# Kernel optimization log

Measured on AMD Instinct MI355X. Metric: run time of the kernel, lower is better.

Reference implementation:

```python
import jax, jax.numpy as jnp
import numpy as np

N_NODES = 100000
N_EDGES = 1600000
D_IN = 128
D_OUT = 128


def setup_inputs() -> dict:
    key = jax.random.key(0)
    k = jax.random.split(key, 7)
    x = jax.random.normal(k[0], (N_NODES, D_IN), dtype=jnp.float32)
    edge_index = jax.random.randint(k[1], (2, N_EDGES), 0, N_NODES, dtype=jnp.int32)
    # MLP params (PyTorch Linear-style scaling)
    s1 = 1.0 / np.sqrt(D_IN)
    s2 = 1.0 / np.sqrt(D_OUT)
    W1 = jax.random.uniform(k[2], (D_IN, D_OUT), jnp.float32, -s1, s1)
    b1 = jax.random.uniform(k[3], (D_OUT,), jnp.float32, -s1, s1)
    W2 = jax.random.uniform(k[4], (D_OUT, D_OUT), jnp.float32, -s2, s2)
    b2 = jax.random.uniform(k[5], (D_OUT,), jnp.float32, -s2, s2)
    eps = jnp.zeros((), dtype=jnp.float32)  # train_eps=True, init 0
    return {"x": x, "edge_index": edge_index, "W1": W1, "b1": b1, "W2": W2, "b2": b2, "eps": eps}


def reference(x, edge_index, W1, b1, W2, b2, eps):
    src, dst = edge_index[0], edge_index[1]  # flow: source_to_target
    # scatter-add neighbor aggregation: agg[i] = sum_{(j->i)} x[j]
    agg = jax.ops.segment_sum(x[src], dst, num_segments=x.shape[0])  # [N, D_IN]
    h = (1.0 + eps) * x + agg
    # 2-layer MLP: Linear -> ReLU -> Linear
    h = jax.nn.relu(h @ W1 + b1)
    return h @ W2 + b2
```

## Files before the change

### kernel.cpp

```cpp
#include <hip/hip_runtime.h>

#define NN    100000
#define NE    1600000
#define DD    128
#define CAP   64
#define NBKT  391
#define PCAP  4608
#define EPB   4096

typedef float  f4v __attribute__((ext_vector_type(4)));
typedef short  s8v __attribute__((ext_vector_type(8)));
typedef unsigned short u16;
typedef unsigned int   u32;

static __device__ __forceinline__ u16 f2bf(float f) {
    u32 u = __float_as_uint(f);
    return (u16)((u + 0x7fffu + ((u >> 16) & 1u)) >> 16);
}
static __device__ __forceinline__ float blo(u32 p) { return __uint_as_float(p << 16); }
static __device__ __forceinline__ float bhi(u32 p) { return __uint_as_float(p & 0xffff0000u); }

__global__ __launch_bounds__(256) void prep_cvt(
    const float* __restrict__ x,
    const float* __restrict__ W1, const float* __restrict__ W2,
    u32* __restrict__ xbp, u16* __restrict__ img1, u16* __restrict__ img2,
    int* __restrict__ gcnt)
{
    const int b   = blockIdx.x;
    const int tid = threadIdx.x;
    if (b < 25000) {
        const int row  = b * 4 + (tid >> 6);
        const int lane = tid & 63;
        const float* xp = x + (size_t)row * DD;
        xbp[(size_t)row * 64 + lane] =
            (u32)f2bf(xp[lane]) | ((u32)f2bf(xp[lane + 64]) << 16);
    } else if (b < 25008) {
        const int gid  = (b - 25000) * 256 + tid;
        const int frag = gid >> 6;
        const int lane = gid & 63;
        const int n  = (frag >> 2) * 16 + (lane & 15);
        const int k0 = (frag & 3) * 32 + (lane >> 4) * 8;
        u16* o1 = img1 + (size_t)gid * 8;
        u16* o2 = img2 + (size_t)gid * 8;
#pragma unroll
        for (int j = 0; j < 8; ++j) {
            o1[j] = f2bf(W1[(size_t)(k0 + j) * DD + n]);
            o2[j] = f2bf(W2[(size_t)(k0 + j) * DD + n]);
        }
    } else if (b < 25033) {
        const int i = (b - 25008) * 256 + tid;
        if (i < NBKT * 16) gcnt[i] = 0;
    } else {
        if (tid < 64) xbp[(size_t)NN * 64 + tid] = 0;
    }
}

__global__ __launch_bounds__(256) void part_kernel(
    const int* __restrict__ ei, u32* __restrict__ pairs, int* __restrict__ gcnt)
{
    __shared__ int hist[NBKT];
    __shared__ int base[NBKT];
    const int tid = threadIdx.x;
    const int e0  = blockIdx.x * EPB;

    int sv[16], dv[16];
#pragma unroll
    for (int t = 0; t < 16; ++t) {
        const int e = e0 + t * 256 + tid;
        if (e < NE) { sv[t] = ei[e]; dv[t] = ei[NE + e]; }
        else        { dv[t] = -1; sv[t] = 0; }
    }

    for (int i = tid; i < NBKT; i += 256) hist[i] = 0;
    __syncthreads();

#pragma unroll
    for (int t = 0; t < 16; ++t)
        if (dv[t] >= 0) atomicAdd(&hist[dv[t] >> 8], 1);
    __syncthreads();

    for (int i = tid; i < NBKT; i += 256) {
        const int h = hist[i];
        base[i] = h ? atomicAdd(&gcnt[i * 16], h) : 0;
        hist[i] = 0;
    }
    __syncthreads();

#pragma unroll
    for (int t = 0; t < 16; ++t)
        if (dv[t] >= 0) {
            const int bk = dv[t] >> 8;
            const int r  = base[bk] + atomicAdd(&hist[bk], 1);
            if (r < PCAP)
                pairs[(size_t)bk * PCAP + r] = ((u32)sv[t] << 8) | (u32)(dv[t] & 255);
        }
}

__global__ __launch_bounds__(256) void build_kernel(
    const u32* __restrict__ pairs, const int* __restrict__ gcnt,
    int* __restrict__ cnt, int* __restrict__ eidx)
{
    __shared__ int cl[256], cur[256];
    const int b   = blockIdx.x;
    const int tid = threadIdx.x;
    const int n   = min(gcnt[b * 16], PCAP);
    const u32* pp = pairs + (size_t)b * PCAP;

    u32 pv[18];
#pragma unroll
    for (int t = 0; t < 18; ++t) {
        const int i = t * 256 + tid;
        if (i < n) pv[t] = pp[i];
    }

    cl[tid] = 0; cur[tid] = 0;
    __syncthreads();

#pragma unroll
    for (int t = 0; t < 18; ++t) {
        const int i = t * 256 + tid;
        if (i < n) atomicAdd(&cl[pv[t] & 255], 1);
    }
    __syncthreads();

    const int g = b * 256 + tid;
    if (g < NN) cnt[g] = cl[tid];

#pragma unroll
    for (int t = 0; t < 18; ++t) {
        const int i = t * 256 + tid;
        if (i < n) {
            const u32 p  = pv[t];
            const int ld = p & 255;
            const int r  = atomicAdd(&cur[ld], 1);
            if (r < CAP) eidx[(size_t)(b * 256 + ld) * CAP + r] = (int)(p >> 8);
        }
    }
}

__global__ __launch_bounds__(256) void gather_kernel(
    const u32* __restrict__ xbp, const int* __restrict__ cnt,
    const int* __restrict__ eidx, const float* __restrict__ epsp,
    u16* __restrict__ hb)
{
    const int node = blockIdx.x * 4 + (threadIdx.x >> 6);
    const int lane = threadIdx.x & 63;
    const int deg  = min(cnt[node], CAP);

    int idxv = eidx[(size_t)node * CAP + lane];
    if (lane >= deg) idxv = NN;

    float a[4] = {}, c[4] = {};

    auto batch16 = [&](int j) {
        u32 p[16];
#pragma unroll
        for (int t = 0; t < 16; ++t) {
            const int s = __builtin_amdgcn_readlane(idxv, j + t);
            const u32* row = xbp + ((size_t)(u32)s << 6);
            p[t] = row[lane];
        }
#pragma unroll
        for (int t = 0; t < 16; ++t) { a[t & 3] += blo(p[t]); c[t & 3] += bhi(p[t]); }
    };
    auto batch8 = [&](int j) {
        u32 p[8];
#pragma unroll
        for (int t = 0; t < 8; ++t) {
            const int s = __builtin_amdgcn_readlane(idxv, j + t);
            const u32* row = xbp + ((size_t)(u32)s << 6);
            p[t] = row[lane];
        }
#pragma unroll
        for (int t = 0; t < 8; ++t) { a[t & 3] += blo(p[t]); c[t & 3] += bhi(p[t]); }
    };

    int j = 0;
    for (; j + 16 <= deg; j += 16) batch16(j);
    const int rem = deg - j;
    if (rem > 0) {
        if (rem <= 8) batch8(j);
        else          batch16(j);
    }

    const float sc = 1.0f + epsp[0];
    const u32 ps = xbp[(size_t)node * 64 + lane];
    const float r0 = sc * blo(ps) + ((a[0] + a[1]) + (a[2] + a[3]));
    const float r1 = sc * bhi(ps) + ((c[0] + c[1]) + (c[2] + c[3]));
    hb[(size_t)node * DD + lane]      = f2bf(r0);
    hb[(size_t)node * DD + lane + 64] = f2bf(r1);
}

__global__ __launch_bounds__(256) void mlp_kernel(
    const u16* __restrict__ hb,
    const u16* __restrict__ img1, const u16* __restrict__ img2,
    const float* __restrict__ b1, const float* __restrict__ b2,
    float* __restrict__ out)
{
    __shared__ char lds_raw[4 * 8448];
    const int tid  = threadIdx.x;
    const int wave = tid >> 6;
    const int lane = tid & 63;
    const int l15  = lane & 15;
    const int quad = lane >> 4;

    float* fstage = (float*)(lds_raw + wave * 8448);
    u16*   hstage = (u16*)fstage;

    int rbase = (blockIdx.x * 4 + wave) * 16;
    if (rbase > NN - 16) rbase = NN - 16;

    float bv1[8], bv2[8];
#pragma unroll
    for (int nt = 0; nt < 8; ++nt) {
        bv1[nt] = b1[nt * 16 + l15];
        bv2[nt] = b2[nt * 16 + l15];
    }

    s8v afrag[4];
#pragma unroll
    for (int kc = 0; kc < 4; ++kc)
        afrag[kc] = *(const s8v*)(hb + (size_t)(rbase + l15) * DD + kc * 32 + quad * 8);

    f4v acc1[8] = {};
#pragma unroll
    for (int kc = 0; kc < 4; ++kc)
#pragma unroll
        for (int nt = 0; nt < 8; ++nt) {
            const s8v bfr = *(const s8v*)(img1 + ((size_t)((nt * 4 + kc) * 64 + lane)) * 8);
            acc1[nt] = __builtin_amdgcn_mfma_f32_16x16x32_bf16(afrag[kc], bfr, acc1[nt], 0, 0, 0);
        }

#pragma unroll
    for (int nt = 0; nt < 8; ++nt)
#pragma unroll
        for (int r = 0; r < 4; ++r) {
            const float v = fmaxf(acc1[nt][r] + bv1[nt], 0.0f);
            hstage[(quad * 4 + r) * 136 + nt * 16 + l15] = f2bf(v);
        }
    __syncthreads();

    s8v a2[4];
#pragma unroll
    for (int kc = 0; kc < 4; ++kc)
        a2[kc] = *(const s8v*)&hstage[l15 * 136 + kc * 32 + quad * 8];

    f4v acc2[8] = {};
#pragma unroll
    for (int kc = 0; kc < 4; ++kc)
#pragma unroll
        for (int nt = 0; nt < 8; ++nt) {
            const s8v bfr = *(const s8v*)(img2 + ((size_t)((nt * 4 + kc) * 64 + lane)) * 8);
            acc2[nt] = __builtin_amdgcn_mfma_f32_16x16x32_bf16(a2[kc], bfr, acc2[nt], 0, 0, 0);
        }

    __syncthreads();
#pragma unroll
    for (int nt = 0; nt < 8; ++nt)
#pragma unroll
        for (int r = 0; r < 4; ++r)
            fstage[(quad * 4 + r) * 132 + nt * 16 + l15] = acc2[nt][r] + bv2[nt];
    __syncthreads();

#pragma unroll
    for (int i = 0; i < 8; ++i) {
        const int m  = (lane >> 5) + 2 * i;
        const int c4 = lane & 31;
        const f4v v = *(const f4v*)&fstage[m * 132 + c4 * 4];
        *(f4v*)(out + (size_t)(rbase + m) * DD + c4 * 4) = v;
    }
}

extern "C" void kernel_launch(void* const* d_in, const int* in_sizes, int n_in,
                              void* d_out, int out_size, void* d_ws, size_t ws_size,
                              hipStream_t stream) {
    const float* x   = (const float*)d_in[0];
    const int*   ei  = (const int*)d_in[1];
    const float* W1  = (const float*)d_in[2];
    const float* b1  = (const float*)d_in[3];
    const float* W2  = (const float*)d_in[4];
    const float* b2  = (const float*)d_in[5];
    const float* eps = (const float*)d_in[6];
    float* out = (float*)d_out;

    u32* xbp   = (u32*)d_ws;
    u16* hb    = (u16*)(xbp + (size_t)(NN + 1) * 64);
    int* eidx  = (int*)(hb + (size_t)NN * DD);
    int* cnt   = eidx + (size_t)NN * CAP;
    u16* img1  = (u16*)(cnt + NN);
    u16* img2  = img1 + (size_t)DD * DD;
    u32* pairs = (u32*)(img2 + (size_t)DD * DD);
    int* gcnt  = (int*)(pairs + (size_t)NBKT * PCAP);

    prep_cvt     <<<25034,              256, 0, stream>>>(x, W1, W2, xbp, img1, img2, gcnt);
    part_kernel  <<<(NE + EPB - 1)/EPB, 256, 0, stream>>>(ei, pairs, gcnt);
    build_kernel <<<NBKT,               256, 0, stream>>>(pairs, gcnt, cnt, eidx);
    gather_kernel<<<NN / 4,             256, 0, stream>>>(xbp, cnt, eidx, eps, hb);
    mlp_kernel   <<<(NN / 16 + 3) / 4,  256, 0, stream>>>(hb, img1, img2, b1, b2, out);
}
```

Measured before the change: 228.5 us.

## Fuse edge partitioning into prep kernel and restructure gather loads

Merges the conversion and edge-partition kernels into one launch, with the bucket-counter zeroing moved to a hipMemsetAsync. The two kernels' blocks can then run concurrently and one launch boundary goes away. The gather kernel now issues up to 32 neighbor loads before accumulating, uses scalarized node and degree values, and adds a launch-bounds occupancy hint. Holding more loads in flight per wave costs extra registers, which may clash with the occupancy target.

```diff
diff --git a/kernel.cpp b/kernel.cpp
--- a/kernel.cpp
+++ b/kernel.cpp
@@ -9,6 +9,7 @@
 #define EPB   4096
 
 typedef float  f4v __attribute__((ext_vector_type(4)));
+typedef float  f2v __attribute__((ext_vector_type(2)));
 typedef short  s8v __attribute__((ext_vector_type(8)));
 typedef unsigned short u16;
 typedef unsigned int   u32;
@@ -17,15 +18,22 @@
     u32 u = __float_as_uint(f);
     return (u16)((u + 0x7fffu + ((u >> 16) & 1u)) >> 16);
 }
-static __device__ __forceinline__ float blo(u32 p) { return __uint_as_float(p << 16); }
-static __device__ __forceinline__ float bhi(u32 p) { return __uint_as_float(p & 0xffff0000u); }
-
-__global__ __launch_bounds__(256) void prep_cvt(
+static __device__ __forceinline__ f2v unpk(u32 p) {
+    f2v r;
+    r.x = __uint_as_float(p << 16);
+    r.y = __uint_as_float(p & 0xffff0000u);
+    return r;
+}
+
+__global__ __launch_bounds__(256) void prep_part(
     const float* __restrict__ x,
     const float* __restrict__ W1, const float* __restrict__ W2,
+    const int* __restrict__ ei,
     u32* __restrict__ xbp, u16* __restrict__ img1, u16* __restrict__ img2,
-    int* __restrict__ gcnt)
+    u32* __restrict__ pairs, int* __restrict__ gcnt)
 {
+    __shared__ int hist[NBKT];
+    __shared__ int base[NBKT];
     const int b   = blockIdx.x;
     const int tid = threadIdx.x;
     if (b < 25000) {
@@ -47,53 +55,43 @@
             o1[j] = f2bf(W1[(size_t)(k0 + j) * DD + n]);
             o2[j] = f2bf(W2[(size_t)(k0 + j) * DD + n]);
         }
-    } else if (b < 25033) {
-        const int i = (b - 25008) * 256 + tid;
-        if (i < NBKT * 16) gcnt[i] = 0;
+    } else if (b == 25008) {
+        if (tid < 64) xbp[(size_t)NN * 64 + tid] = 0;
     } else {
-        if (tid < 64) xbp[(size_t)NN * 64 + tid] = 0;
-    }
-}
-
-__global__ __launch_bounds__(256) void part_kernel(
-    const int* __restrict__ ei, u32* __restrict__ pairs, int* __restrict__ gcnt)
-{
-    __shared__ int hist[NBKT];
-    __shared__ int base[NBKT];
-    const int tid = threadIdx.x;
-    const int e0  = blockIdx.x * EPB;
-
-    int sv[16], dv[16];
-#pragma unroll
-    for (int t = 0; t < 16; ++t) {
-        const int e = e0 + t * 256 + tid;
-        if (e < NE) { sv[t] = ei[e]; dv[t] = ei[NE + e]; }
-        else        { dv[t] = -1; sv[t] = 0; }
-    }
-
-    for (int i = tid; i < NBKT; i += 256) hist[i] = 0;
-    __syncthreads();
-
-#pragma unroll
-    for (int t = 0; t < 16; ++t)
-        if (dv[t] >= 0) atomicAdd(&hist[dv[t] >> 8], 1);
-    __syncthreads();
-
-    for (int i = tid; i < NBKT; i += 256) {
-        const int h = hist[i];
-        base[i] = h ? atomicAdd(&gcnt[i * 16], h) : 0;
-        hist[i] = 0;
-    }
-    __syncthreads();
-
-#pragma unroll
-    for (int t = 0; t < 16; ++t)
-        if (dv[t] >= 0) {
-            const int bk = dv[t] >> 8;
-            const int r  = base[bk] + atomicAdd(&hist[bk], 1);
-            if (r < PCAP)
-                pairs[(size_t)bk * PCAP + r] = ((u32)sv[t] << 8) | (u32)(dv[t] & 255);
-        }
+        const int e0 = (b - 25009) * EPB;
+
+        int sv[16], dv[16];
+#pragma unroll
+        for (int t = 0; t < 16; ++t) {
+            const int e = e0 + t * 256 + tid;
+            if (e < NE) { sv[t] = ei[e]; dv[t] = ei[NE + e]; }
+            else        { dv[t] = -1; sv[t] = 0; }
+        }
+
+        for (int i = tid; i < NBKT; i += 256) hist[i] = 0;
+        __syncthreads();
+
+#pragma unroll
+        for (int t = 0; t < 16; ++t)
+            if (dv[t] >= 0) atomicAdd(&hist[dv[t] >> 8], 1);
+        __syncthreads();
+
+        for (int i = tid; i < NBKT; i += 256) {
+            const int h = hist[i];
+            base[i] = h ? atomicAdd(&gcnt[i * 16], h) : 0;
+            hist[i] = 0;
+        }
+        __syncthreads();
+
+#pragma unroll
+        for (int t = 0; t < 16; ++t)
+            if (dv[t] >= 0) {
+                const int bk = dv[t] >> 8;
+                const int r  = base[bk] + atomicAdd(&hist[bk], 1);
+                if (r < PCAP)
+                    pairs[(size_t)bk * PCAP + r] = ((u32)sv[t] << 8) | (u32)(dv[t] & 255);
+            }
+    }
 }
 
 __global__ __launch_bounds__(256) void build_kernel(
@@ -138,57 +136,64 @@
     }
 }
 
-__global__ __launch_bounds__(256) void gather_kernel(
+__global__ __launch_bounds__(256, 8) void gather_kernel(
     const u32* __restrict__ xbp, const int* __restrict__ cnt,
     const int* __restrict__ eidx, const float* __restrict__ epsp,
     u16* __restrict__ hb)
 {
-    const int node = blockIdx.x * 4 + (threadIdx.x >> 6);
-    const int lane = threadIdx.x & 63;
-    const int deg  = min(cnt[node], CAP);
-
-    int idxv = eidx[(size_t)node * CAP + lane];
+    const int node  = blockIdx.x * 4 + (threadIdx.x >> 6);
+    const int lane  = threadIdx.x & 63;
+    const int noded = __builtin_amdgcn_readfirstlane(node);
+
+    const u32   ps = xbp[((size_t)noded << 6) + lane];
+    const float sc = 1.0f + epsp[0];
+
+    const int deg = __builtin_amdgcn_readfirstlane(min(cnt[noded], CAP));
+    int idxv = eidx[((size_t)noded << 6) + lane];
     if (lane >= deg) idxv = NN;
 
-    float a[4] = {}, c[4] = {};
-
-    auto batch16 = [&](int j) {
-        u32 p[16];
+    f2v acc[4] = {};
+    u32 p[32];
+    const int nb = (deg + 15) >> 4;
+
+    if (nb > 0) {
 #pragma unroll
         for (int t = 0; t < 16; ++t) {
-            const int s = __builtin_amdgcn_readlane(idxv, j + t);
-            const u32* row = xbp + ((size_t)(u32)s << 6);
-            p[t] = row[lane];
-        }
-#pragma unroll
-        for (int t = 0; t < 16; ++t) { a[t & 3] += blo(p[t]); c[t & 3] += bhi(p[t]); }
-    };
-    auto batch8 = [&](int j) {
-        u32 p[8];
-#pragma unroll
-        for (int t = 0; t < 8; ++t) {
-            const int s = __builtin_amdgcn_readlane(idxv, j + t);
-            const u32* row = xbp + ((size_t)(u32)s << 6);
-            p[t] = row[lane];
-        }
-#pragma unroll
-        for (int t = 0; t < 8; ++t) { a[t & 3] += blo(p[t]); c[t & 3] += bhi(p[t]); }
-    };
-
-    int j = 0;
-    for (; j + 16 <= deg; j += 16) batch16(j);
-    const int rem = deg - j;
-    if (rem > 0) {
-        if (rem <= 8) batch8(j);
-        else          batch16(j);
-    }
-
-    const float sc = 1.0f + epsp[0];
-    const u32 ps = xbp[(size_t)node * 64 + lane];
-    const float r0 = sc * blo(ps) + ((a[0] + a[1]) + (a[2] + a[3]));
-    const float r1 = sc * bhi(ps) + ((c[0] + c[1]) + (c[2] + c[3]));
-    hb[(size_t)node * DD + lane]      = f2bf(r0);
-    hb[(size_t)node * DD + lane + 64] = f2bf(r1);
+            const u32 s = (u32)__builtin_amdgcn_readlane(idxv, t);
+            p[t] = xbp[((size_t)s << 6) + lane];
+        }
+    }
+    if (nb > 1) {
+#pragma unroll
+        for (int t = 0; t < 16; ++t) {
+            const u32 s = (u32)__builtin_amdgcn_readlane(idxv, 16 + t);
+            p[16 + t] = xbp[((size_t)s << 6) + lane];
+        }
+    }
+    if (nb > 0) {
+#pragma unroll
+        for (int t = 0; t < 16; ++t) acc[t & 3] += unpk(p[t]);
+    }
+    if (nb > 1) {
+#pragma unroll
+        for (int t = 0; t < 16; ++t) acc[t & 3] += unpk(p[16 + t]);
+    }
+    for (int b = 2; b < nb; ++b) {
+#pragma unroll
+        for (int t = 0; t < 16; ++t) {
+            const u32 s = (u32)__builtin_amdgcn_readlane(idxv, b * 16 + t);
+            p[t] = xbp[((size_t)s << 6) + lane];
+        }
+#pragma unroll
+        for (int t = 0; t < 16; ++t) acc[t & 3] += unpk(p[t]);
+    }
+
+    const f2v s01 = acc[0] + acc[1];
+    const f2v s23 = acc[2] + acc[3];
+    const f2v st  = s01 + s23;
+    const f2v sv  = unpk(ps);
+    hb[(size_t)noded * DD + lane]      = f2bf(fmaf(sc, sv.x, st.x));
+    hb[(size_t)noded * DD + lane + 64] = f2bf(fmaf(sc, sv.y, st.y));
 }
 
 __global__ __launch_bounds__(256) void mlp_kernel(
@@ -292,9 +297,9 @@
     u32* pairs = (u32*)(img2 + (size_t)DD * DD);
     int* gcnt  = (int*)(pairs + (size_t)NBKT * PCAP);
 
-    prep_cvt     <<<25034,              256, 0, stream>>>(x, W1, W2, xbp, img1, img2, gcnt);
-    part_kernel  <<<(NE + EPB - 1)/EPB, 256, 0, stream>>>(ei, pairs, gcnt);
-    build_kernel <<<NBKT,               256, 0, stream>>>(pairs, gcnt, cnt, eidx);
-    gather_kernel<<<NN / 4,             256, 0, stream>>>(xbp, cnt, eidx, eps, hb);
-    mlp_kernel   <<<(NN / 16 + 3) / 4,  256, 0, stream>>>(hb, img1, img2, b1, b2, out);
-}
+    hipMemsetAsync(gcnt, 0, (size_t)NBKT * 16 * sizeof(int), stream);
+    prep_part    <<<25400,             256, 0, stream>>>(x, W1, W2, ei, xbp, img1, img2, pairs, gcnt);
+    build_kernel <<<NBKT,              256, 0, stream>>>(pairs, gcnt, cnt, eidx);
+    gather_kernel<<<NN / 4,            256, 0, stream>>>(xbp, cnt, eidx, eps, hb);
+    mlp_kernel   <<<(NN / 16 + 3) / 4, 256, 0, stream>>>(hb, img1, img2, b1, b2, out);
+}
```

New measurement: 235.4 us. 3.0% more time.
